# Kernel tuning notes

Hardware: AMD Instinct MI355X
Metric: run time of the kernel (lower is better)

## Reference

```python
import jax, jax.numpy as jnp
import numpy as np

VAR0, VAR1 = 0.1, 0.2      # cfg['variance'] standard SSD values
THRESH = 0.5               # overlap_thresh
NEG_POS = 3                # negpos_ratio


def point_form(p):
    # (cx,cy,w,h) -> (xmin,ymin,xmax,ymax)
    return jnp.concatenate([p[:, :2] - p[:, 2:] / 2, p[:, :2] + p[:, 2:] / 2], axis=1)


def jaccard(a, b):
    # a: [n,4] corner boxes, b: [P,4] corner boxes -> IoU [n,P]
    lt = jnp.maximum(a[:, None, :2], b[None, :, :2])
    rb = jnp.minimum(a[:, None, 2:], b[None, :, 2:])
    wh = jnp.clip(rb - lt, 0.0)
    inter = wh[..., 0] * wh[..., 1]
    area_a = (a[:, 2] - a[:, 0]) * (a[:, 3] - a[:, 1])
    area_b = (b[:, 2] - b[:, 0]) * (b[:, 3] - b[:, 1])
    return inter / (area_a[:, None] + area_b[None, :] - inter + 1e-10)


def encode(matched, priors):
    # matched: [P,4] corner form GT, priors: [P,4] center form
    g_cxcy = ((matched[:, :2] + matched[:, 2:]) / 2 - priors[:, :2]) / (VAR0 * priors[:, 2:])
    g_wh = jnp.log((matched[:, 2:] - matched[:, :2]) / priors[:, 2:] + 1e-10) / VAR1
    return jnp.concatenate([g_cxcy, g_wh], axis=1)


def match_one(truths, labels, priors_cw, priors_pf):
    # truths: [n,4] corner, labels: [n] float
    n = truths.shape[0]
    overlaps = jaccard(truths, priors_pf)                 # [n,P]
    best_prior_idx = jnp.argmax(overlaps, axis=1)         # [n]
    best_truth_overlap = jnp.max(overlaps, axis=0)        # [P]
    best_truth_idx = jnp.argmax(overlaps, axis=0)         # [P]
    # ensure each GT keeps its best prior
    best_truth_overlap = best_truth_overlap.at[best_prior_idx].set(2.0)
    best_truth_idx = best_truth_idx.at[best_prior_idx].set(jnp.arange(n))
    matched = truths[best_truth_idx]                      # [P,4]
    conf = (labels[best_truth_idx] + 1.0).astype(jnp.int32)
    conf = jnp.where(best_truth_overlap < THRESH, 0, conf)
    loc_t = encode(matched, priors_cw)
    return loc_t, conf


def setup_inputs() -> dict:
    key = jax.random.key(0)
    k1, k2, k3, k4, k5, k6 = jax.random.split(key, 6)
    B, P, C, NOBJ = 64, 24564, 81, 16
    loc_data = jax.random.normal(k1, (B, P, 4), dtype=jnp.float32)
    conf_data = jax.random.normal(k2, (B, P, C), dtype=jnp.float32)
    # priors in (cx,cy,w,h) form, realistic sizes
    pc = jax.random.uniform(k3, (P, 2), minval=0.05, maxval=0.95)
    pw = jax.random.uniform(k4, (P, 2), minval=0.05, maxval=0.5)
    priors = jnp.concatenate([pc, pw], axis=1).astype(jnp.float32)
    # targets: corner-form GT boxes + label in last column
    c = jax.random.uniform(k5, (B, NOBJ, 2), minval=0.15, maxval=0.85)
    s = jax.random.uniform(k6, (B, NOBJ, 2), minval=0.05, maxval=0.4)
    boxes = jnp.concatenate([jnp.clip(c - s / 2, 0.0, 1.0), jnp.clip(c + s / 2, 0.0, 1.0)], axis=-1)
    labels = jax.random.randint(jax.random.fold_in(key, 7), (B, NOBJ, 1), 0, C - 1).astype(jnp.float32)
    targets = jnp.concatenate([boxes, labels], axis=-1).astype(jnp.float32)
    return {"loc_data": loc_data, "conf_data": conf_data, "priors": priors, "targets": targets}


def reference(loc_data, conf_data, priors, targets):
    B, P, C = conf_data.shape
    priors_pf = point_form(priors)
    truths = targets[..., :4]
    labels = targets[..., 4]
    loc_t, conf_t = jax.vmap(lambda t, l: match_one(t, l, priors, priors_pf))(truths, labels)
    pos = conf_t > 0                                       # [B,P]
    # localization loss: smooth L1 over positives
    d = jnp.abs(loc_data - loc_t)
    sl1 = jnp.where(d < 1.0, 0.5 * d * d, d - 0.5)
    loss_l = jnp.sum(sl1 * pos[..., None].astype(sl1.dtype))
    # confidence loss with hard negative mining
    lse = jax.nn.logsumexp(conf_data, axis=-1)             # [B,P]
    gathered = jnp.take_along_axis(conf_data, conf_t[..., None], axis=-1)[..., 0]
    ce = lse - gathered                                    # [B,P]
    ce_mine = jnp.where(pos, 0.0, ce)
    loss_idx = jnp.argsort(-ce_mine, axis=1)
    idx_rank = jnp.argsort(loss_idx, axis=1)
    num_pos = jnp.sum(pos, axis=1, keepdims=True)          # [B,1]
    num_neg = jnp.minimum(NEG_POS * num_pos, P - 1)
    neg = idx_rank < num_neg
    mask = pos | neg
    loss_c = jnp.sum(jnp.where(mask, ce, 0.0))
    N = jnp.maximum(jnp.sum(num_pos), 1).astype(loss_l.dtype)
    return jnp.stack([loss_l / N, loss_c / N])
```

## Files before the change

kernel.cpp:

```cpp
#include <hip/hip_runtime.h>
#include <cstdint>
#include <cstddef>

#define THRESH_F 0.5f
#define VAR0_F 0.1f
#define VAR1_F 0.2f
#define NEG_POS_K 3
#define MAXOBJ 64

__global__ void init_kernel(unsigned long long* __restrict__ bp_packed, int nbp,
                            unsigned int* __restrict__ hist_g, int nh,
                            unsigned int* __restrict__ sel_done) {
    int i = blockIdx.x * blockDim.x + threadIdx.x;
    if (i < nbp) bp_packed[i] = 0ull;
    if (i < nh) hist_g[i] = 0u;
    if (i == 0) *sel_done = 0u;
}

__global__ __launch_bounds__(256)
void fused_kernel(const float* __restrict__ priors,
                  const float* __restrict__ targets,
                  const float* __restrict__ conf,
                  uchar2* __restrict__ clsti,
                  unsigned long long* __restrict__ bp_packed,
                  float2* __restrict__ lse_c0,
                  int P, int NOBJ, int mgx, int nMatch, int NBX) {
    int bid = blockIdx.x;
    int tid = threadIdx.x;
    int lane = tid & 63;

    if (bid < nMatch) {
        int b = bid / mgx;
        int mbx = bid - b * mgx;
        int p = mbx * 256 + tid;
        bool valid = (p < P);
        __shared__ float tx1[MAXOBJ], ty1[MAXOBJ], tx2[MAXOBJ], ty2[MAXOBJ], ta[MAXOBJ], tl[MAXOBJ];
        __shared__ unsigned long long smax[MAXOBJ];
        if (tid < (unsigned)NOBJ) {
            const float* t = targets + ((size_t)b * NOBJ + tid) * 5;
            float x1 = t[0], y1 = t[1], x2 = t[2], y2 = t[3];
            tx1[tid] = x1; ty1[tid] = y1;
            tx2[tid] = x2; ty2[tid] = y2;
            ta[tid] = (x2 - x1) * (y2 - y1);
            tl[tid] = t[4];
            smax[tid] = 0ull;
        }
        __syncthreads();

        int pc = valid ? p : (P - 1);
        const float4 prv = *(const float4*)(priors + (size_t)pc * 4);
        float cx = prv.x, cy = prv.y, w = prv.z, h = prv.w;
        float px1 = cx - w * 0.5f, py1 = cy - h * 0.5f;
        float px2 = cx + w * 0.5f, py2 = cy + h * 0.5f;
        float pa = (px2 - px1) * (py2 - py1);
        float best = -1.0f; int bidx = 0;

        for (int t = 0; t < NOBJ; ++t) {
            float lx = fmaxf(tx1[t], px1), ly = fmaxf(ty1[t], py1);
            float rx = fminf(tx2[t], px2), ry = fminf(ty2[t], py2);
            float iw = fmaxf(rx - lx, 0.0f), ih = fmaxf(ry - ly, 0.0f);
            float inter = iw * ih;
            float iou = inter / ((ta[t] + pa) - inter + 1e-10f);
            float iouv = valid ? iou : -1.0f;
            if (iouv > best) { best = iouv; bidx = t; }
            float wm = iouv;
            #pragma unroll
            for (int o = 32; o > 0; o >>= 1) wm = fmaxf(wm, __shfl_xor(wm, o, 64));
            unsigned long long eq = __ballot(iouv == wm);
            int src = (int)__ffsll(eq) - 1;
            if (lane == src && valid) {
                unsigned long long pk = ((unsigned long long)__float_as_uint(iouv) << 32)
                                      | (unsigned long long)(0xFFFFFFFFu - (unsigned)p);
                if (pk > smax[t]) atomicMax(&smax[t], pk);
            }
        }
        if (valid) {
            int cls = (best >= THRESH_F) ? (int)(tl[bidx] + 1.0f) : 0;
            clsti[(size_t)b * P + p] = make_uchar2((unsigned char)cls, (unsigned char)bidx);
        }
        __syncthreads();
        if (tid < (unsigned)NOBJ) {
            unsigned long long v = smax[tid];
            unsigned long long* dst = &bp_packed[(size_t)b * NOBJ + tid];
            if (v > *dst) atomicMax(dst, v);
        }
    } else {
        int cb = bid - nMatch;
        int b = cb / NBX;
        int blkx = cb - b * NBX;
        int wid = tid >> 6;
        int q = lane >> 4;
        int lq = lane & 15;
        int p = blkx * 16 + wid * 4 + q;
        if (p >= P) return;
        size_t row = (size_t)b * P + p;
        size_t rowStartF = row * 81;

        size_t alignedF = rowStartF & ~(size_t)3;
        int r = (int)(rowStartF & 3);
        const float4* w4 = (const float4*)(conf + alignedF);

        float4 vA = w4[lq];
        bool hasB = (lq < 5);
        float4 vB = hasB ? w4[16 + lq] : vA;

        float s = 0.0f;
        {
            int e0 = 4 * lq;
            s += (e0 + 0 >= r) ? __expf(vA.x) : 0.0f;
            s += (e0 + 1 >= r) ? __expf(vA.y) : 0.0f;
            s += (e0 + 2 >= r) ? __expf(vA.z) : 0.0f;
            s += (e0 + 3 >= r) ? __expf(vA.w) : 0.0f;
        }
        if (hasB) {
            int e0 = 64 + 4 * lq;
            int hi = 81 + r;
            s += (e0 + 0 < hi) ? __expf(vB.x) : 0.0f;
            s += (e0 + 1 < hi) ? __expf(vB.y) : 0.0f;
            s += (e0 + 2 < hi) ? __expf(vB.z) : 0.0f;
            s += (e0 + 3 < hi) ? __expf(vB.w) : 0.0f;
        }
        #pragma unroll
        for (int o = 8; o > 0; o >>= 1) s += __shfl_xor(s, o, 64);

        if (lq == 0) {
            float c0 = (r == 0) ? vA.x : (r == 1) ? vA.y : (r == 2) ? vA.z : vA.w;
            lse_c0[row] = make_float2(__logf(s), c0);
        }
    }
}

__global__ __launch_bounds__(256)
void epilogue_kernel(const float* __restrict__ loc,
                     const float* __restrict__ conf,
                     const float* __restrict__ priors,
                     const float* __restrict__ targets,
                     const uchar2* __restrict__ clsti,
                     const unsigned long long* __restrict__ bp_packed,
                     const float2* __restrict__ lse_c0,
                     float* __restrict__ ce_mine,
                     float* __restrict__ part_np,
                     float* __restrict__ part_ce,
                     float* __restrict__ part_ll,
                     unsigned int* __restrict__ hist_g,
                     int P, int NOBJ) {
    int tid = threadIdx.x;
    int lane = tid & 63;
    int wid = tid >> 6;
    int p = blockIdx.x * 256 + tid;
    int b = blockIdx.y;
    bool active = (p < P);
    size_t row = (size_t)b * P + p;

    __shared__ unsigned shist[256];
    __shared__ unsigned sp[MAXOBJ];
    __shared__ unsigned char scls[MAXOBJ];
    __shared__ float s_np[4], s_ce[4], s_ll[4];
    shist[tid] = 0u;
    if (tid < (unsigned)NOBJ) {
        unsigned long long pk = bp_packed[(size_t)b * NOBJ + tid];
        sp[tid] = 0xFFFFFFFFu - (unsigned)(pk & 0xFFFFFFFFull);
        scls[tid] = (unsigned char)(targets[((size_t)b * NOBJ + tid) * 5 + 4] + 1.0f);
    }
    __syncthreads();

    float cnt = 0.0f, ces = 0.0f, lls = 0.0f;
    float cm = 0.0f;

    if (active) {
        float2 lc = lse_c0[row];
        int fj = -1;
        #pragma unroll
        for (int j = 0; j < 16; ++j)
            if (j < NOBJ && sp[j] == (unsigned)p) fj = j;
        int cls, ti;
        if (fj >= 0) { cls = scls[fj]; ti = fj; }
        else { uchar2 ct = clsti[row]; cls = ct.x; ti = ct.y; }

        float gathered = (cls == 0) ? lc.y : conf[row * 81 + cls];
        float ce = lc.x - gathered;
        bool pos = cls > 0;
        cm = pos ? 0.0f : fmaxf(ce, 0.0f);
        ce_mine[row] = cm;
        if (pos) {
            cnt = 1.0f;
            ces = ce;
            const float* tb = targets + ((size_t)b * NOBJ + ti) * 5;
            const float4 prv = *(const float4*)(priors + (size_t)p * 4);
            float pcx = prv.x, pcy = prv.y, pw = prv.z, ph = prv.w;
            float m0 = tb[0], m1 = tb[1], m2 = tb[2], m3 = tb[3];
            float g0 = ((m0 + m2) * 0.5f - pcx) / (VAR0_F * pw);
            float g1 = ((m1 + m3) * 0.5f - pcy) / (VAR0_F * ph);
            float g2 = __logf((m2 - m0) / pw + 1e-10f) / VAR1_F;
            float g3 = __logf((m3 - m1) / ph + 1e-10f) / VAR1_F;
            float g[4] = {g0, g1, g2, g3};
            const float4 lv = *(const float4*)(loc + row * 4);
            float l[4] = {lv.x, lv.y, lv.z, lv.w};
            float acc = 0.0f;
            #pragma unroll
            for (int d = 0; d < 4; ++d) {
                float diff = fabsf(l[d] - g[d]);
                acc += (diff < 1.0f) ? 0.5f * diff * diff : diff - 0.5f;
            }
            lls = acc;
        }
    }

    {
        unsigned d = __float_as_uint(cm) >> 24;
        bool pred = active;
        unsigned long long act = __ballot(pred);
        while (act) {
            int leader = (int)__ffsll(act) - 1;
            unsigned dl = (unsigned)__shfl((int)d, leader, 64);
            unsigned long long same = __ballot(pred && (d == dl));
            if (lane == leader) atomicAdd(&shist[dl], (unsigned)__popcll(same));
            act &= ~same;
        }
    }

    #pragma unroll
    for (int o = 32; o > 0; o >>= 1) {
        cnt += __shfl_xor(cnt, o, 64);
        ces += __shfl_xor(ces, o, 64);
        lls += __shfl_xor(lls, o, 64);
    }
    if (lane == 0) { s_np[wid] = cnt; s_ce[wid] = ces; s_ll[wid] = lls; }
    __syncthreads();
    if (tid == 0) {
        size_t idx = (size_t)b * gridDim.x + blockIdx.x;
        part_np[idx] = s_np[0] + s_np[1] + s_np[2] + s_np[3];
        part_ce[idx] = s_ce[0] + s_ce[1] + s_ce[2] + s_ce[3];
        part_ll[idx] = s_ll[0] + s_ll[1] + s_ll[2] + s_ll[3];
    }
    unsigned hv = shist[tid];
    if (hv > 0) atomicAdd(&hist_g[(size_t)b * 256 + tid], hv);
}

__device__ inline double blockReduceD(double v, double* sd) {
    __syncthreads();
    #pragma unroll
    for (int o = 32; o > 0; o >>= 1) v += __shfl_xor(v, o, 64);
    int wid = threadIdx.x >> 6, lane = threadIdx.x & 63;
    if (lane == 0) sd[wid] = v;
    __syncthreads();
    if (threadIdx.x == 0) {
        double t = 0.0; int nw = blockDim.x >> 6;
        for (int i = 0; i < nw; ++i) t += sd[i];
        sd[0] = t;
    }
    __syncthreads();
    return sd[0];
}

__device__ inline double agent_load_d(const double* p) {
    unsigned long long v = __hip_atomic_load((const unsigned long long*)p,
                                             __ATOMIC_RELAXED, __HIP_MEMORY_SCOPE_AGENT);
    return __longlong_as_double((long long)v);
}

__global__ __launch_bounds__(1024)
void select_kernel(const float* __restrict__ ce_mine,
                   const float* __restrict__ part_np,
                   const float* __restrict__ part_ce,
                   const float* __restrict__ part_ll,
                   const unsigned int* __restrict__ hist_g,
                   double* __restrict__ np_b,
                   double* __restrict__ lc_b,
                   double* __restrict__ ll_b,
                   unsigned int* __restrict__ done_cnt,
                   float* __restrict__ out,
                   int P, int NBX, int B) {
    int b = blockIdx.x;
    int tid = threadIdx.x;
    __shared__ unsigned int hist[256];
    __shared__ unsigned int s_prefix;
    __shared__ int s_krem;
    __shared__ double sd[16];
    __shared__ bool s_last;

    double np_f = 0.0, ce_f = 0.0, ll_f = 0.0;
    for (int i = tid; i < NBX; i += blockDim.x) {
        size_t ix = (size_t)b * NBX + i;
        np_f += (double)part_np[ix];
        ce_f += (double)part_ce[ix];
        ll_f += (double)part_ll[ix];
    }
    double np_d = blockReduceD(np_f, sd);
    double ce_sum = blockReduceD(ce_f, sd);
    double ll_sum = blockReduceD(ll_f, sd);

    int np = (int)(np_d + 0.5);
    long long k = (long long)NEG_POS_K * np;
    if (k > P - 1) k = P - 1;

    if (k <= 0) {
        if (tid == 0) { np_b[b] = (double)np; lc_b[b] = ce_sum; ll_b[b] = ll_sum; }
    } else {
        const float* vals = ce_mine + (size_t)b * P;
        const float4* v4 = (const float4*)vals;
        int nq = P >> 2;
        unsigned prefix = 0;
        int krem = (int)k;

        {
            const unsigned int* hg = hist_g + (size_t)b * 256;
            if (tid < 64) {
                unsigned c0 = hg[4 * tid], c1 = hg[4 * tid + 1];
                unsigned c2 = hg[4 * tid + 2], c3 = hg[4 * tid + 3];
                unsigned lsum = c0 + c1 + c2 + c3;
                unsigned suf = lsum;
                #pragma unroll
                for (int o = 1; o < 64; o <<= 1) {
                    unsigned other = (unsigned)__shfl_down((int)suf, o, 64);
                    if (tid + o < 64) suf += other;
                }
                unsigned suffAfter = suf - lsum;
                unsigned K = (unsigned)krem;
                if (suf >= K && suffAfter < K) {
                    unsigned s3 = c3 + suffAfter;
                    unsigned s2 = c2 + s3;
                    unsigned s1 = c1 + s2;
                    int dloc; unsigned above;
                    if (s3 >= K)      { dloc = 3; above = suffAfter; }
                    else if (s2 >= K) { dloc = 2; above = s3; }
                    else if (s1 >= K) { dloc = 1; above = s2; }
                    else              { dloc = 0; above = s1; }
                    s_prefix = (unsigned)(4 * tid + dloc) << 24;
                    s_krem = (int)(K - above);
                }
            }
            __syncthreads();
            prefix = s_prefix;
            krem = s_krem;
            __syncthreads();
        }

        for (int pass = 1; pass < 4; ++pass) {
            int shift = 24 - 8 * pass;
            unsigned mask_hi = 0xFFFFFFFFu << (shift + 8);
            if (tid < 256) hist[tid] = 0;
            __syncthreads();
            for (int i = tid; i < nq; i += blockDim.x) {
                float4 v = v4[i];
                unsigned k0 = __float_as_uint(v.x), k1 = __float_as_uint(v.y);
                unsigned k2 = __float_as_uint(v.z), k3 = __float_as_uint(v.w);
                if ((k0 & mask_hi) == prefix) atomicAdd(&hist[(k0 >> shift) & 255], 1u);
                if ((k1 & mask_hi) == prefix) atomicAdd(&hist[(k1 >> shift) & 255], 1u);
                if ((k2 & mask_hi) == prefix) atomicAdd(&hist[(k2 >> shift) & 255], 1u);
                if ((k3 & mask_hi) == prefix) atomicAdd(&hist[(k3 >> shift) & 255], 1u);
            }
            for (int i = (nq << 2) + tid; i < P; i += blockDim.x) {
                unsigned key = __float_as_uint(vals[i]);
                if ((key & mask_hi) == prefix)
                    atomicAdd(&hist[(key >> shift) & 255], 1u);
            }
            __syncthreads();
            if (tid < 64) {
                unsigned c0 = hist[4 * tid], c1 = hist[4 * tid + 1];
                unsigned c2 = hist[4 * tid + 2], c3 = hist[4 * tid + 3];
                unsigned lsum = c0 + c1 + c2 + c3;
                unsigned suf = lsum;
                #pragma unroll
                for (int o = 1; o < 64; o <<= 1) {
                    unsigned other = (unsigned)__shfl_down((int)suf, o, 64);
                    if (tid + o < 64) suf += other;
                }
                unsigned suffAfter = suf - lsum;
                unsigned K = (unsigned)krem;
                if (suf >= K && suffAfter < K) {
                    unsigned s3 = c3 + suffAfter;
                    unsigned s2 = c2 + s3;
                    unsigned s1 = c1 + s2;
                    int dloc; unsigned above;
                    if (s3 >= K)      { dloc = 3; above = suffAfter; }
                    else if (s2 >= K) { dloc = 2; above = s3; }
                    else if (s1 >= K) { dloc = 1; above = s2; }
                    else              { dloc = 0; above = s1; }
                    s_prefix = prefix | ((unsigned)(4 * tid + dloc) << shift);
                    s_krem = (int)(K - above);
                }
            }
            __syncthreads();
            prefix = s_prefix;
            krem = s_krem;
            __syncthreads();
        }

        unsigned tbits = prefix;
        double mysum = 0.0;
        for (int i = tid; i < nq; i += blockDim.x) {
            float4 v = v4[i];
            if (__float_as_uint(v.x) > tbits) mysum += (double)v.x;
            if (__float_as_uint(v.y) > tbits) mysum += (double)v.y;
            if (__float_as_uint(v.z) > tbits) mysum += (double)v.z;
            if (__float_as_uint(v.w) > tbits) mysum += (double)v.w;
        }
        for (int i = (nq << 2) + tid; i < P; i += blockDim.x) {
            float v = vals[i];
            if (__float_as_uint(v) > tbits) mysum += (double)v;
        }
        double selsum = blockReduceD(mysum, sd);
        if (tid == 0) {
            np_b[b] = (double)np;
            lc_b[b] = ce_sum + selsum + (double)krem * (double)__uint_as_float(tbits);
            ll_b[b] = ll_sum;
        }
    }

    if (tid == 0) {
        __threadfence();
        unsigned old = atomicAdd(done_cnt, 1u);
        s_last = (old == gridDim.x - 1);
    }
    __syncthreads();
    if (s_last) {
        __threadfence();
        if (tid < 64) {
            double np2 = 0.0, lc2 = 0.0, ll2 = 0.0;
            for (int i = tid; i < B; i += 64) {
                np2 += agent_load_d(np_b + i);
                lc2 += agent_load_d(lc_b + i);
                ll2 += agent_load_d(ll_b + i);
            }
            #pragma unroll
            for (int o = 32; o > 0; o >>= 1) {
                np2 += __shfl_xor(np2, o, 64);
                lc2 += __shfl_xor(lc2, o, 64);
                ll2 += __shfl_xor(ll2, o, 64);
            }
            if (tid == 0) {
                double N = np2 > 0.0 ? np2 : 1.0;
                out[0] = (float)(ll2 / N);
                out[1] = (float)(lc2 / N);
            }
        }
    }
}

extern "C" void kernel_launch(void* const* d_in, const int* in_sizes, int n_in,
                              void* d_out, int out_size, void* d_ws, size_t ws_size,
                              hipStream_t stream) {
    const float* loc     = (const float*)d_in[0];
    const float* conf    = (const float*)d_in[1];
    const float* priors  = (const float*)d_in[2];
    const float* targets = (const float*)d_in[3];

    int P = in_sizes[2] / 4;
    long long nloc = in_sizes[0];
    int B = (int)(nloc / ((long long)P * 4));
    int C = (int)((long long)in_sizes[1] / ((long long)B * P));
    int NOBJ = in_sizes[3] / (B * 5);
    (void)C;
    int NBX = (P + 15) / 16;
    int mgx = (P + 255) / 256;
    int NBE = (P + 255) / 256;

    size_t BP = (size_t)B * P;
    auto align256 = [](size_t x) { return (x + 255) & ~(size_t)255; };
    size_t off = 0;
    uchar2* clsti = (uchar2*)((char*)d_ws + off);             off = align256(off + BP * 2);
    float* ce_mine = (float*)((char*)d_ws + off);             off = align256(off + BP * 4);
    float2* lse_c0 = (float2*)((char*)d_ws + off);            off = align256(off + BP * 8);
    unsigned long long* bp_packed = (unsigned long long*)((char*)d_ws + off); off = align256(off + (size_t)B * NOBJ * 8);
    float* part_np = (float*)((char*)d_ws + off);             off = align256(off + (size_t)B * NBE * 4);
    float* part_ce = (float*)((char*)d_ws + off);             off = align256(off + (size_t)B * NBE * 4);
    float* part_ll = (float*)((char*)d_ws + off);             off = align256(off + (size_t)B * NBE * 4);
    unsigned int* hist_g = (unsigned int*)((char*)d_ws + off); off = align256(off + (size_t)B * 256 * 4);
    double* np_b = (double*)((char*)d_ws + off);              off = align256(off + (size_t)B * 8);
    double* lc_b = (double*)((char*)d_ws + off);              off = align256(off + (size_t)B * 8);
    double* ll_b = (double*)((char*)d_ws + off);              off = align256(off + (size_t)B * 8);
    unsigned int* sel_done = (unsigned int*)((char*)d_ws + off); off = align256(off + 4);

    float* out = (float*)d_out;

    int nbp = B * NOBJ;
    int nh = B * 256;
    int ninit = nh > nbp ? nh : nbp;
    init_kernel<<<(ninit + 255) / 256, 256, 0, stream>>>(bp_packed, nbp, hist_g, nh, sel_done);

    int nMatch = mgx * B;
    int nLse = NBX * B;
    fused_kernel<<<nMatch + nLse, 256, 0, stream>>>(priors, targets, conf,
                                                    clsti, bp_packed, lse_c0,
                                                    P, NOBJ, mgx, nMatch, NBX);

    dim3 egrid(NBE, B);
    epilogue_kernel<<<egrid, 256, 0, stream>>>(loc, conf, priors, targets, clsti,
                                               bp_packed, lse_c0, ce_mine,
                                               part_np, part_ce, part_ll, hist_g, P, NOBJ);

    select_kernel<<<B, 1024, 0, stream>>>(ce_mine, part_np, part_ce, part_ll, hist_g,
                                          np_b, lc_b, ll_b, sel_done, out, P, NBE, B);
}
```

Before: 214.9 us.

## Stream conf rows as contiguous float4 tiles with shared-memory atomic row sums

The logsumexp branch now has each block cover 64 rows. It streams their contiguous 81-float chunks as aligned float4 loads spread across all threads, instead of one 16-lane group per row making misaligned partial loads. Row sums are accumulated with shared-memory atomics, using a multiply-shift divide by 81 to find the row, and class-0 logits are captured on the fly. This is meant to give fully coalesced reads and fewer wasted lanes, at the cost of LDS atomic contention and one fewer block per 16 rows. It also assumes each block's start (b*P+rowBase)*81 is 16-byte aligned, which holds because 64*81 is divisible by 4 and P is even.

```diff
diff --git a/kernel.cpp b/kernel.cpp
--- a/kernel.cpp
+++ b/kernel.cpp
@@ -7,6 +7,7 @@
 #define VAR1_F 0.2f
 #define NEG_POS_K 3
 #define MAXOBJ 64
+#define LSE_ROWS 64
 
 __global__ void init_kernel(unsigned long long* __restrict__ bp_packed, int nbp,
                             unsigned int* __restrict__ hist_g, int nh,
@@ -88,44 +89,52 @@
         int cb = bid - nMatch;
         int b = cb / NBX;
         int blkx = cb - b * NBX;
-        int wid = tid >> 6;
-        int q = lane >> 4;
-        int lq = lane & 15;
-        int p = blkx * 16 + wid * 4 + q;
-        if (p >= P) return;
-        size_t row = (size_t)b * P + p;
-        size_t rowStartF = row * 81;
-
-        size_t alignedF = rowStartF & ~(size_t)3;
-        int r = (int)(rowStartF & 3);
-        const float4* w4 = (const float4*)(conf + alignedF);
-
-        float4 vA = w4[lq];
-        bool hasB = (lq < 5);
-        float4 vB = hasB ? w4[16 + lq] : vA;
-
-        float s = 0.0f;
-        {
-            int e0 = 4 * lq;
-            s += (e0 + 0 >= r) ? __expf(vA.x) : 0.0f;
-            s += (e0 + 1 >= r) ? __expf(vA.y) : 0.0f;
-            s += (e0 + 2 >= r) ? __expf(vA.z) : 0.0f;
-            s += (e0 + 3 >= r) ? __expf(vA.w) : 0.0f;
-        }
-        if (hasB) {
-            int e0 = 64 + 4 * lq;
-            int hi = 81 + r;
-            s += (e0 + 0 < hi) ? __expf(vB.x) : 0.0f;
-            s += (e0 + 1 < hi) ? __expf(vB.y) : 0.0f;
-            s += (e0 + 2 < hi) ? __expf(vB.z) : 0.0f;
-            s += (e0 + 3 < hi) ? __expf(vB.w) : 0.0f;
-        }
-        #pragma unroll
-        for (int o = 8; o > 0; o >>= 1) s += __shfl_xor(s, o, 64);
-
-        if (lq == 0) {
-            float c0 = (r == 0) ? vA.x : (r == 1) ? vA.y : (r == 2) ? vA.z : vA.w;
-            lse_c0[row] = make_float2(__logf(s), c0);
+        int rowBase = blkx * LSE_ROWS;
+        int rows = P - rowBase;
+        if (rows > LSE_ROWS) rows = LSE_ROWS;
+
+        __shared__ float ssum[LSE_ROWS];
+        __shared__ float sc0[LSE_ROWS];
+        if (tid < LSE_ROWS) ssum[tid] = 0.0f;
+        __syncthreads();
+
+        const float* gf = conf + ((size_t)b * P + rowBase) * 81;
+        const float4* g4 = (const float4*)gf;
+        int nf = rows * 81;
+        int nf4 = nf >> 2;
+
+        for (int i = tid; i < nf4; i += 256) {
+            float4 v = g4[i];
+            int e0 = i << 2;
+            int r = (int)(((unsigned)e0 * 12946u) >> 20);
+            int j = e0 - r * 81;
+            float ex = __expf(v.x), ey = __expf(v.y);
+            float ez = __expf(v.z), ew = __expf(v.w);
+            if (j <= 77) {
+                atomicAdd(&ssum[r], (ex + ey) + (ez + ew));
+            } else {
+                int nIn = 81 - j;
+                float s1 = ex + (nIn > 1 ? ey : 0.0f) + (nIn > 2 ? ez : 0.0f);
+                float s2 = (nIn <= 1 ? ey : 0.0f) + (nIn <= 2 ? ez : 0.0f) + ew;
+                atomicAdd(&ssum[r], s1);
+                atomicAdd(&ssum[r + 1], s2);
+            }
+            if (j == 0)       sc0[r] = v.x;
+            else if (j == 78) sc0[r + 1] = v.w;
+            else if (j == 79) sc0[r + 1] = v.z;
+            else if (j == 80) sc0[r + 1] = v.y;
+        }
+        for (int e = (nf4 << 2) + tid; e < nf; e += 256) {
+            float v = gf[e];
+            int r = (int)(((unsigned)e * 12946u) >> 20);
+            int j = e - r * 81;
+            atomicAdd(&ssum[r], __expf(v));
+            if (j == 0) sc0[r] = v;
+        }
+        __syncthreads();
+        if (tid < rows) {
+            size_t row = (size_t)b * P + rowBase + tid;
+            lse_c0[row] = make_float2(__logf(ssum[tid]), sc0[tid]);
         }
     }
 }
@@ -452,7 +461,7 @@
     int C = (int)((long long)in_sizes[1] / ((long long)B * P));
     int NOBJ = in_sizes[3] / (B * 5);
     (void)C;
-    int NBX = (P + 15) / 16;
+    int NBX = (P + LSE_ROWS - 1) / LSE_ROWS;
     int mgx = (P + 255) / 256;
     int NBE = (P + 255) / 256;
 
```

Result: slower. 311.5 us (+44.9%).
